# Kernel tuning notes

Hardware: AMD Instinct MI355X
Metric: run time of the kernel (lower is better)

Reference implementation:

```python
import jax, jax.numpy as jnp
import numpy as np

SEQ_LEN = 2048
EMBED_DIM = 1024
NUM_HEADS = 16
DIM_HEAD = EMBED_DIM // NUM_HEADS
BATCH = 4


def setup_inputs() -> dict:
    key = jax.random.key(0)
    k1, k2, k3 = jax.random.split(key, 3)
    x = jax.random.normal(k1, (SEQ_LEN, BATCH, EMBED_DIM), dtype=jnp.float32)
    weight_qkv = jax.random.normal(k2, (3 * EMBED_DIM, EMBED_DIM), dtype=jnp.float32) * (EMBED_DIM ** -0.5)
    weight_out = jax.random.normal(k3, (EMBED_DIM, EMBED_DIM), dtype=jnp.float32) * (EMBED_DIM ** -0.5)
    # causal mask: True where attention is DISALLOWED (strict upper triangle)
    mask = ~jnp.tril(jnp.ones((SEQ_LEN, SEQ_LEN), dtype=bool))[None, None]  # [1,1,L,L]
    return {"x": x, "weight_qkv": weight_qkv, "weight_out": weight_out, "mask": mask}


def reference(x, weight_qkv, weight_out, mask):
    L, N, E = x.shape
    H, Dh = NUM_HEADS, DIM_HEAD
    scale = Dh ** -0.5
    qkv = x @ weight_qkv.T                       # [L, N, 3E]
    q, k, v = jnp.split(qkv, 3, axis=-1)         # each [L, N, E]
    # [L, N, E] -> [N*H, L, Dh]
    def to_heads(t):
        return t.reshape(L, N * H, Dh).transpose(1, 0, 2)
    q, k, v = to_heads(q) * scale, to_heads(k), to_heads(v)
    attn = jnp.einsum('bld,bmd->blm', q, k)      # [N*H, L, L]
    attn = attn.reshape(N, H, L, L)
    attn = jnp.where(mask, jnp.float32(-100000.0), attn)
    attn = jax.nn.softmax(attn.reshape(N * H, L, L), axis=-1)
    out = jnp.einsum('blm,bmd->bld', attn, v)    # [N*H, L, Dh]
    out = out.transpose(1, 0, 2).reshape(L, N, E)
    return out @ weight_out.T
```

## Files before the change

kernel.cpp:

```cpp
#include <hip/hip_runtime.h>
#include <hip/hip_bf16.h>
#include <stdint.h>

constexpr int L  = 2048;
constexpr int NB = 4;
constexpr int E  = 1024;
constexpr int H  = 16;
constexpr int M  = L * NB;
constexpr int K  = E;
constexpr int QKV_LD = 3 * E;

typedef float  f32x4  __attribute__((ext_vector_type(4)));
typedef float  f32x16 __attribute__((ext_vector_type(16)));
typedef __bf16 bf16x4 __attribute__((ext_vector_type(4)));
typedef __bf16 bf16x8 __attribute__((ext_vector_type(8)));

#define AS1 __attribute__((address_space(1)))
#define AS3 __attribute__((address_space(3)))

static __device__ __forceinline__ void gl_lds16(const void* g, void* l) {
  __builtin_amdgcn_global_load_lds((const AS1 uint32_t*)g, (AS3 uint32_t*)l, 16, 0, 0);
}

__global__ __launch_bounds__(256)
void cvt_f32_bf16(const float* __restrict__ in, __bf16* __restrict__ out, int n4) {
  const int i = blockIdx.x * blockDim.x + threadIdx.x;
  if (i < n4) {
    const f32x4 v = ((const f32x4*)in)[i];
    bf16x4 o;
#pragma unroll
    for (int j = 0; j < 4; j++) o[j] = (__bf16)v[j];
    ((bf16x4*)out)[i] = o;
  }
}

template<int NC, typename OutT>
__global__ __launch_bounds__(256)
void gemm_bt(const __bf16* __restrict__ A, const __bf16* __restrict__ B,
             OutT* __restrict__ C) {
  constexpr int BK = 64;
  __shared__ char lds[2 * 128 * BK * 2];
  char* aL = lds;
  char* bL = lds + 128 * BK * 2;

  const int t    = threadIdx.x;
  const int lane = t & 63;
  const int w    = t >> 6;
  const int g    = lane >> 4;
  const int c    = lane & 15;

  const int nwg = gridDim.x * gridDim.y;
  const int lin = blockIdx.x + gridDim.x * blockIdx.y;
  const int q8  = nwg >> 3;
  const int swz = (lin & 7) * q8 + (lin >> 3);
  const int bx  = swz % gridDim.x;
  const int by  = swz / gridDim.x;

  const int rowBase = by * 128;
  const int colBase = bx * 128;

  const int srow = t >> 3;
  const int scb  = (t & 7) * 16;
  const int ssw  = scb ^ ((srow & 7) << 4);

  const char* aSrcBase = (const char*)(A + (size_t)(rowBase + srow) * K) + ssw;
  const char* bSrcBase = (const char*)(B + (size_t)(colBase + srow) * K) + ssw;

  f32x4 acc[4][4];
#pragma unroll
  for (int i = 0; i < 4; i++)
#pragma unroll
    for (int j = 0; j < 4; j++) acc[i][j] = f32x4{0.f, 0.f, 0.f, 0.f};

  const int wr = (w >> 1) * 64;
  const int wc = (w & 1) * 64;

  for (int k0 = 0; k0 < K; k0 += BK) {
    __syncthreads();
#pragma unroll
    for (int q = 0; q < 4; q++) {
      gl_lds16(aSrcBase + (size_t)2 * k0 + (size_t)q * 32 * K * 2, aL + q * 4096 + t * 16);
      gl_lds16(bSrcBase + (size_t)2 * k0 + (size_t)q * 32 * K * 2, bL + q * 4096 + t * 16);
    }
    __syncthreads();

    bf16x8 af[4][2], bfR[4][2];
#pragma unroll
    for (int mi = 0; mi < 4; mi++) {
      const int row = wr + mi * 16 + c;
      const int sw  = (row & 7) << 4;
#pragma unroll
      for (int ks = 0; ks < 2; ks++)
        af[mi][ks] = *(const bf16x8*)(aL + row * 128 + ((ks * 64 + g * 16) ^ sw));
    }
#pragma unroll
    for (int ni = 0; ni < 4; ni++) {
      const int row = wc + ni * 16 + c;
      const int sw  = (row & 7) << 4;
#pragma unroll
      for (int ks = 0; ks < 2; ks++)
        bfR[ni][ks] = *(const bf16x8*)(bL + row * 128 + ((ks * 64 + g * 16) ^ sw));
    }
#pragma unroll
    for (int mi = 0; mi < 4; mi++)
#pragma unroll
      for (int ni = 0; ni < 4; ni++)
#pragma unroll
        for (int ks = 0; ks < 2; ks++)
          acc[mi][ni] = __builtin_amdgcn_mfma_f32_16x16x32_bf16(
              af[mi][ks], bfR[ni][ks], acc[mi][ni], 0, 0, 0);
  }

#pragma unroll
  for (int mi = 0; mi < 4; mi++)
#pragma unroll
    for (int ni = 0; ni < 4; ni++)
#pragma unroll
      for (int r = 0; r < 4; r++) {
        const int row = rowBase + wr + mi * 16 + g * 4 + r;
        const int col = colBase + wc + ni * 16 + c;
        C[(size_t)row * NC + col] = (OutT)acc[mi][ni][r];
      }
}

__global__ __launch_bounds__(256)
void transpose_v(const __bf16* __restrict__ qkv, __bf16* __restrict__ vT) {
  __shared__ char tile[64 * 160];
  const int lt = blockIdx.x;
  const int bh = blockIdx.y;
  const int n  = bh >> 4, h = bh & 15;
  const int t  = threadIdx.x;
  const int r8 = t >> 3;
  const int c8 = (t & 7) * 8;

#pragma unroll
  for (int q2 = 0; q2 < 2; q2++) {
    const int l = q2 * 32 + r8;
    const bf16x8 v = *(const bf16x8*)(qkv + (size_t)((lt * 64 + l) * 4 + n) * QKV_LD +
                                      2 * E + h * 64 + c8);
    *(bf16x8*)(tile + l * 160 + ((c8 * 2) ^ (((l >> 3) & 7) << 4))) = v;
  }
  __syncthreads();
#pragma unroll
  for (int q2 = 0; q2 < 2; q2++) {
    const int d = q2 * 32 + r8;
    bf16x8 o;
#pragma unroll
    for (int i = 0; i < 8; i++) {
      const int l = c8 + i;
      o[i] = *(const __bf16*)(tile + l * 160 + ((d * 2) ^ (((l >> 3) & 7) << 4)));
    }
    *(bf16x8*)(vT + ((size_t)bh * 64 + d) * 2048 + lt * 64 + c8) = o;
  }
}

__global__ __launch_bounds__(256)
void attn_kernel(const __bf16* __restrict__ qkv, const __bf16* __restrict__ vT,
                 __bf16* __restrict__ out) {
  const int b  = blockIdx.x;
  const int qx = blockIdx.y;
  const int n  = b >> 4;
  const int h  = b & 15;

  __shared__ char kl[2][64 * 128];
  __shared__ char vl[2][64 * 128];
  __shared__ char pl[4][32 * 128];

  const int t    = threadIdx.x;
  const int lane = t & 63;
  const int w    = t >> 6;
  const int l31  = lane & 31;
  const int hi   = lane >> 5;

  const int srow = t >> 3;
  const int scb  = (t & 7) * 16;
  int kssw[2];
#pragma unroll
  for (int q2 = 0; q2 < 2; q2++) {
    const int row = q2 * 32 + srow;
    kssw[q2] = scb ^ (((row ^ (row >> 3)) & 7) << 4);
  }

  const int krow0 = l31,      sw0 = ((krow0 ^ (krow0 >> 3)) & 7) << 4;
  const int krow1 = 32 + l31, sw1 = ((krow1 ^ (krow1 >> 3)) & 7) << 4;

  constexpr float QSCALE = 0.125f * 1.4426950408889634f;

  const int qt    = (w < 2) ? qx : 31 - qx;
  const int qh    = w & 1;
  const int ktEnd = 31 - qx;
  const int qg    = qt * 64 + qh * 32 + l31;

  char* pw = pl[w];

  bf16x8 qb[4];
  {
    const __bf16* qp = qkv + (size_t)(qg * 4 + n) * QKV_LD + h * 64;
#pragma unroll
    for (int ds = 0; ds < 4; ds++) {
      qb[ds] = *(const bf16x8*)(qp + ds * 16 + hi * 8);
#pragma unroll
      for (int i = 0; i < 8; i++) qb[ds][i] = (__bf16)((float)qb[ds][i] * QSCALE);
    }
  }

  float m_c = -3e38f, l_c = 0.f;
  f32x16 o0, o1;
#pragma unroll
  for (int j = 0; j < 16; j++) { o0[j] = 0.f; o1[j] = 0.f; }

  int cur = 0;

#pragma unroll
  for (int q2 = 0; q2 < 2; q2++) {
    const int kvrow = q2 * 32 + srow;
    gl_lds16((const char*)(qkv + (size_t)(kvrow * 4 + n) * QKV_LD + E + h * 64) + kssw[q2],
             kl[0] + q2 * 4096 + t * 16);
    gl_lds16((const char*)(vT + ((size_t)b * 64 + kvrow) * 2048) + kssw[q2],
             vl[0] + q2 * 4096 + t * 16);
  }

  for (int kt = 0; kt <= ktEnd; ++kt) {
    __syncthreads();

    if (kt < ktEnd) {
      const int nx = kt + 1;
#pragma unroll
      for (int q2 = 0; q2 < 2; q2++) {
        const int kvrow = nx * 64 + q2 * 32 + srow;
        gl_lds16((const char*)(qkv + (size_t)(kvrow * 4 + n) * QKV_LD + E + h * 64) + kssw[q2],
                 kl[cur ^ 1] + q2 * 4096 + t * 16);
        const int vd = q2 * 32 + srow;
        gl_lds16((const char*)(vT + ((size_t)b * 64 + vd) * 2048 + nx * 64) + kssw[q2],
                 vl[cur ^ 1] + q2 * 4096 + t * 16);
      }
    }
    __builtin_amdgcn_sched_barrier(0);

    if (kt <= qt) {
      const char* klc = kl[cur];
      const char* vlc = vl[cur];

      f32x16 s0, s1;
#pragma unroll
      for (int j = 0; j < 16; j++) { s0[j] = 0.f; s1[j] = 0.f; }
      __builtin_amdgcn_s_setprio(1);
#pragma unroll
      for (int ds = 0; ds < 4; ds++) {
        const int col = ds * 32 + hi * 16;
        const bf16x8 ka0 = *(const bf16x8*)(klc + krow0 * 128 + (col ^ sw0));
        const bf16x8 ka1 = *(const bf16x8*)(klc + krow1 * 128 + (col ^ sw1));
        s0 = __builtin_amdgcn_mfma_f32_32x32x16_bf16(ka0, qb[ds], s0, 0, 0, 0);
        s1 = __builtin_amdgcn_mfma_f32_32x32x16_bf16(ka1, qb[ds], s1, 0, 0, 0);
      }
      __builtin_amdgcn_s_setprio(0);

      if (kt == qt) {
#pragma unroll
        for (int reg = 0; reg < 16; reg++) {
          const int kvp = (reg & 3) + 8 * (reg >> 2) + 4 * hi;
          if (kt * 64 + kvp      > qg) s0[reg] = -1e30f;
          if (kt * 64 + 32 + kvp > qg) s1[reg] = -1e30f;
        }
      }

      float rmax = s0[0];
#pragma unroll
      for (int reg = 1; reg < 16; reg++) rmax = fmaxf(rmax, s0[reg]);
#pragma unroll
      for (int reg = 0; reg < 16; reg++) rmax = fmaxf(rmax, s1[reg]);
      rmax = fmaxf(rmax, __shfl_xor(rmax, 32));

      if (__any(rmax > m_c + 8.f)) {
        const float mnew  = fmaxf(m_c, rmax);
        const float alpha = exp2f(m_c - mnew);
        l_c *= alpha;
#pragma unroll
        for (int reg = 0; reg < 16; reg++) {
          const int   qp = (reg & 3) + 8 * (reg >> 2) + 4 * hi;
          const float ar = __shfl(alpha, qp);
          o0[reg] *= ar;
          o1[reg] *= ar;
        }
        m_c = mnew;
      }

      float rsum = 0.f;
#pragma unroll
      for (int reg = 0; reg < 16; reg++) {
        const float e0 = exp2f(s0[reg] - m_c);
        const float e1 = exp2f(s1[reg] - m_c);
        s0[reg] = e0; s1[reg] = e1;
        rsum += e0 + e1;
      }
      rsum += __shfl_xor(rsum, 32);
      l_c += rsum;

#pragma unroll
      for (int rg = 0; rg < 8; rg++) {
        bf16x4 pk;
#pragma unroll
        for (int j = 0; j < 4; j++)
          pk[j] = (__bf16)((rg < 4) ? s0[(rg & 3) * 4 + j] : s1[(rg & 3) * 4 + j]);
        const int kvb = (rg & 3) * 16 + hi * 8 + (rg >> 2) * 64;
        *(bf16x4*)(pw + l31 * 128 + (kvb ^ sw0)) = pk;
      }

#pragma unroll
      for (int s_ = 0; s_ < 4; s_++) {
        const int colp = s_ * 32 + hi * 16;
        const bf16x8 pa  = *(const bf16x8*)(pw + l31 * 128 + (colp ^ sw0));
        const bf16x8 vb0 = *(const bf16x8*)(vlc + krow0 * 128 + (colp ^ sw0));
        const bf16x8 vb1 = *(const bf16x8*)(vlc + krow1 * 128 + (colp ^ sw1));
        __builtin_amdgcn_s_setprio(1);
        o0 = __builtin_amdgcn_mfma_f32_32x32x16_bf16(pa, vb0, o0, 0, 0, 0);
        o1 = __builtin_amdgcn_mfma_f32_32x32x16_bf16(pa, vb1, o1, 0, 0, 0);
        __builtin_amdgcn_s_setprio(0);
      }
    }

    cur ^= 1;
  }

  const float inv = 1.f / l_c;
#pragma unroll
  for (int reg = 0; reg < 16; reg++) {
    const int   qp  = (reg & 3) + 8 * (reg >> 2) + 4 * hi;
    const float li  = __shfl(inv, qp);
    const int   qrw = qt * 64 + qh * 32 + qp;
    const size_t base = (size_t)(qrw * 4 + n) * E + h * 64;
    out[base + l31]      = (__bf16)(o0[reg] * li);
    out[base + 32 + l31] = (__bf16)(o1[reg] * li);
  }
}

extern "C" void kernel_launch(void* const* d_in, const int* in_sizes, int n_in,
                              void* d_out, int out_size, void* d_ws, size_t ws_size,
                              hipStream_t stream) {
  const float* x    = (const float*)d_in[0];
  const float* wqkv = (const float*)d_in[1];
  const float* wout = (const float*)d_in[2];

  char* ws = (char*)d_ws;
  __bf16* x_bf    = (__bf16*)ws;                         ws += (size_t)M * E * 2;
  __bf16* wqkv_bf = (__bf16*)ws;                         ws += (size_t)QKV_LD * E * 2;
  __bf16* wout_bf = (__bf16*)ws;                         ws += (size_t)E * E * 2;
  __bf16* qkv     = (__bf16*)ws;                         ws += (size_t)M * QKV_LD * 2;
  __bf16* attno   = (__bf16*)ws;
  __bf16* vT      = x_bf;
  float*  outp    = (float*)d_out;

  cvt_f32_bf16<<<(M * E / 4) / 256, 256, 0, stream>>>(x, x_bf, M * E / 4);
  cvt_f32_bf16<<<(QKV_LD * E / 4) / 256, 256, 0, stream>>>(wqkv, wqkv_bf, QKV_LD * E / 4);
  cvt_f32_bf16<<<(E * E / 4) / 256, 256, 0, stream>>>(wout, wout_bf, E * E / 4);

  gemm_bt<QKV_LD, __bf16><<<dim3(QKV_LD / 128, M / 128), 256, 0, stream>>>(x_bf, wqkv_bf, qkv);
  transpose_v<<<dim3(L / 64, NB * H), 256, 0, stream>>>(qkv, vT);
  attn_kernel<<<dim3(NB * H, 16), 256, 0, stream>>>(qkv, vT, attno);
  gemm_bt<E, float><<<dim3(E / 128, M / 128), 256, 0, stream>>>(attno, wout_bf, outp);
}
```

Before: 218.9 us.

## Share K/V tiles across four warps on 128-row query blocks and shuffle P via registers

The attention kernel now gives each block two passes over 128-row query supertiles (y and 15-y), so all four warps work on adjacent query rows and share every loaded K/V tile instead of splitting between two distant 64-row tiles. The grid halves to 8 blocks per head. The softmax probability tile is no longer staged through shared memory; it is rearranged into the MFMA A-operand layout with cross-half-wave shuffles. This cuts redundant K/V loads and LDS traffic, but leaves fewer, longer blocks with a serialized second pass and adds shuffle instructions.

New measurement: 199.0 us. 1.1x faster.

```diff
diff --git a/kernel.cpp b/kernel.cpp
--- a/kernel.cpp
+++ b/kernel.cpp
@@ -14,6 +14,8 @@
 typedef float  f32x16 __attribute__((ext_vector_type(16)));
 typedef __bf16 bf16x4 __attribute__((ext_vector_type(4)));
 typedef __bf16 bf16x8 __attribute__((ext_vector_type(8)));
+typedef unsigned int uint2v __attribute__((ext_vector_type(2)));
+typedef unsigned int uint4v __attribute__((ext_vector_type(4)));
 
 #define AS1 __attribute__((address_space(1)))
 #define AS3 __attribute__((address_space(3)))
@@ -158,13 +160,12 @@
 void attn_kernel(const __bf16* __restrict__ qkv, const __bf16* __restrict__ vT,
                  __bf16* __restrict__ out) {
   const int b  = blockIdx.x;
-  const int qx = blockIdx.y;
+  const int y  = blockIdx.y;
   const int n  = b >> 4;
   const int h  = b & 15;
 
   __shared__ char kl[2][64 * 128];
   __shared__ char vl[2][64 * 128];
-  __shared__ char pl[4][32 * 128];
 
   const int t    = threadIdx.x;
   const int lane = t & 63;
@@ -185,29 +186,6 @@
   const int krow1 = 32 + l31, sw1 = ((krow1 ^ (krow1 >> 3)) & 7) << 4;
 
   constexpr float QSCALE = 0.125f * 1.4426950408889634f;
-
-  const int qt    = (w < 2) ? qx : 31 - qx;
-  const int qh    = w & 1;
-  const int ktEnd = 31 - qx;
-  const int qg    = qt * 64 + qh * 32 + l31;
-
-  char* pw = pl[w];
-
-  bf16x8 qb[4];
-  {
-    const __bf16* qp = qkv + (size_t)(qg * 4 + n) * QKV_LD + h * 64;
-#pragma unroll
-    for (int ds = 0; ds < 4; ds++) {
-      qb[ds] = *(const bf16x8*)(qp + ds * 16 + hi * 8);
-#pragma unroll
-      for (int i = 0; i < 8; i++) qb[ds][i] = (__bf16)((float)qb[ds][i] * QSCALE);
-    }
-  }
-
-  float m_c = -3e38f, l_c = 0.f;
-  f32x16 o0, o1;
-#pragma unroll
-  for (int j = 0; j < 16; j++) { o0[j] = 0.f; o1[j] = 0.f; }
 
   int cur = 0;
 
@@ -220,117 +198,152 @@
              vl[0] + q2 * 4096 + t * 16);
   }
 
-  for (int kt = 0; kt <= ktEnd; ++kt) {
-    __syncthreads();
-
-    if (kt < ktEnd) {
-      const int nx = kt + 1;
-#pragma unroll
-      for (int q2 = 0; q2 < 2; q2++) {
-        const int kvrow = nx * 64 + q2 * 32 + srow;
-        gl_lds16((const char*)(qkv + (size_t)(kvrow * 4 + n) * QKV_LD + E + h * 64) + kssw[q2],
-                 kl[cur ^ 1] + q2 * 4096 + t * 16);
-        const int vd = q2 * 32 + srow;
-        gl_lds16((const char*)(vT + ((size_t)b * 64 + vd) * 2048 + nx * 64) + kssw[q2],
-                 vl[cur ^ 1] + q2 * 4096 + t * 16);
+  for (int pass = 0; pass < 2; ++pass) {
+    const int qsup = pass ? 15 - y : y;
+    const int qb_  = qsup * 128 + w * 32;
+    const int qg   = qb_ + l31;
+    const int ktEnd = 2 * qsup + 1;
+
+    bf16x8 qb[4];
+    {
+      const __bf16* qp = qkv + (size_t)(qg * 4 + n) * QKV_LD + h * 64;
+#pragma unroll
+      for (int ds = 0; ds < 4; ds++) {
+        qb[ds] = *(const bf16x8*)(qp + ds * 16 + hi * 8);
+#pragma unroll
+        for (int i = 0; i < 8; i++) qb[ds][i] = (__bf16)((float)qb[ds][i] * QSCALE);
       }
     }
-    __builtin_amdgcn_sched_barrier(0);
-
-    if (kt <= qt) {
-      const char* klc = kl[cur];
-      const char* vlc = vl[cur];
-
-      f32x16 s0, s1;
-#pragma unroll
-      for (int j = 0; j < 16; j++) { s0[j] = 0.f; s1[j] = 0.f; }
-      __builtin_amdgcn_s_setprio(1);
-#pragma unroll
-      for (int ds = 0; ds < 4; ds++) {
-        const int col = ds * 32 + hi * 16;
-        const bf16x8 ka0 = *(const bf16x8*)(klc + krow0 * 128 + (col ^ sw0));
-        const bf16x8 ka1 = *(const bf16x8*)(klc + krow1 * 128 + (col ^ sw1));
-        s0 = __builtin_amdgcn_mfma_f32_32x32x16_bf16(ka0, qb[ds], s0, 0, 0, 0);
-        s1 = __builtin_amdgcn_mfma_f32_32x32x16_bf16(ka1, qb[ds], s1, 0, 0, 0);
+
+    float m_c = -3e38f, l_c = 0.f;
+    f32x16 o0, o1;
+#pragma unroll
+    for (int j = 0; j < 16; j++) { o0[j] = 0.f; o1[j] = 0.f; }
+
+    for (int kt = 0; kt <= ktEnd; ++kt) {
+      __syncthreads();
+
+      const bool last = (kt == ktEnd);
+      if (!last || pass == 0) {
+        const int nx = last ? 0 : kt + 1;
+#pragma unroll
+        for (int q2 = 0; q2 < 2; q2++) {
+          const int kvrow = nx * 64 + q2 * 32 + srow;
+          gl_lds16((const char*)(qkv + (size_t)(kvrow * 4 + n) * QKV_LD + E + h * 64) + kssw[q2],
+                   kl[cur ^ 1] + q2 * 4096 + t * 16);
+          const int vd = q2 * 32 + srow;
+          gl_lds16((const char*)(vT + ((size_t)b * 64 + vd) * 2048 + nx * 64) + kssw[q2],
+                   vl[cur ^ 1] + q2 * 4096 + t * 16);
+        }
       }
-      __builtin_amdgcn_s_setprio(0);
-
-      if (kt == qt) {
+      __builtin_amdgcn_sched_barrier(0);
+
+      if (kt * 64 <= qb_ + 31) {
+        const char* klc = kl[cur];
+        const char* vlc = vl[cur];
+
+        f32x16 s0, s1;
+#pragma unroll
+        for (int j = 0; j < 16; j++) { s0[j] = 0.f; s1[j] = 0.f; }
+        __builtin_amdgcn_s_setprio(1);
+#pragma unroll
+        for (int ds = 0; ds < 4; ds++) {
+          const int col = ds * 32 + hi * 16;
+          const bf16x8 ka0 = *(const bf16x8*)(klc + krow0 * 128 + (col ^ sw0));
+          const bf16x8 ka1 = *(const bf16x8*)(klc + krow1 * 128 + (col ^ sw1));
+          s0 = __builtin_amdgcn_mfma_f32_32x32x16_bf16(ka0, qb[ds], s0, 0, 0, 0);
+          s1 = __builtin_amdgcn_mfma_f32_32x32x16_bf16(ka1, qb[ds], s1, 0, 0, 0);
+        }
+        __builtin_amdgcn_s_setprio(0);
+
+        if (kt * 64 + 63 > qb_) {
+#pragma unroll
+          for (int reg = 0; reg < 16; reg++) {
+            const int kvp = (reg & 3) + 8 * (reg >> 2) + 4 * hi;
+            if (kt * 64 + kvp      > qg) s0[reg] = -1e30f;
+            if (kt * 64 + 32 + kvp > qg) s1[reg] = -1e30f;
+          }
+        }
+
+        float rmax = s0[0];
+#pragma unroll
+        for (int reg = 1; reg < 16; reg++) rmax = fmaxf(rmax, s0[reg]);
+#pragma unroll
+        for (int reg = 0; reg < 16; reg++) rmax = fmaxf(rmax, s1[reg]);
+        rmax = fmaxf(rmax, __shfl_xor(rmax, 32));
+
+        if (__any(rmax > m_c + 8.f)) {
+          const float mnew  = fmaxf(m_c, rmax);
+          const float alpha = exp2f(m_c - mnew);
+          l_c *= alpha;
+#pragma unroll
+          for (int reg = 0; reg < 16; reg++) {
+            const int   qp = (reg & 3) + 8 * (reg >> 2) + 4 * hi;
+            const float ar = __shfl(alpha, qp);
+            o0[reg] *= ar;
+            o1[reg] *= ar;
+          }
+          m_c = mnew;
+        }
+
+        float rsum = 0.f;
 #pragma unroll
         for (int reg = 0; reg < 16; reg++) {
-          const int kvp = (reg & 3) + 8 * (reg >> 2) + 4 * hi;
-          if (kt * 64 + kvp      > qg) s0[reg] = -1e30f;
-          if (kt * 64 + 32 + kvp > qg) s1[reg] = -1e30f;
+          const float e0 = exp2f(s0[reg] - m_c);
+          const float e1 = exp2f(s1[reg] - m_c);
+          s0[reg] = e0; s1[reg] = e1;
+          rsum += e0 + e1;
+        }
+        rsum += __shfl_xor(rsum, 32);
+        l_c += rsum;
+
+        unsigned int runA[8], runB[8];
+#pragma unroll
+        for (int rg = 0; rg < 8; rg++) {
+          bf16x4 pk;
+#pragma unroll
+          for (int j = 0; j < 4; j++)
+            pk[j] = (__bf16)((rg < 4) ? s0[(rg & 3) * 4 + j] : s1[(rg & 3) * 4 + j]);
+          const uint2v u = *(const uint2v*)&pk;
+          runA[rg] = u[0]; runB[rg] = u[1];
+        }
+
+#pragma unroll
+        for (int s_ = 0; s_ < 4; s_++) {
+          const unsigned int ownA = hi ? runA[2 * s_ + 1] : runA[2 * s_];
+          const unsigned int ownB = hi ? runB[2 * s_ + 1] : runB[2 * s_];
+          const unsigned int sndA = hi ? runA[2 * s_]     : runA[2 * s_ + 1];
+          const unsigned int sndB = hi ? runB[2 * s_]     : runB[2 * s_ + 1];
+          const unsigned int rxA  = (unsigned int)__shfl_xor((int)sndA, 32);
+          const unsigned int rxB  = (unsigned int)__shfl_xor((int)sndB, 32);
+          uint4v pu;
+          pu[0] = hi ? rxA : ownA;  pu[1] = hi ? rxB : ownB;
+          pu[2] = hi ? ownA : rxA;  pu[3] = hi ? ownB : rxB;
+          const bf16x8 pa = *(const bf16x8*)&pu;
+
+          const int colp = s_ * 32 + hi * 16;
+          const bf16x8 vb0 = *(const bf16x8*)(vlc + krow0 * 128 + (colp ^ sw0));
+          const bf16x8 vb1 = *(const bf16x8*)(vlc + krow1 * 128 + (colp ^ sw1));
+          __builtin_amdgcn_s_setprio(1);
+          o0 = __builtin_amdgcn_mfma_f32_32x32x16_bf16(pa, vb0, o0, 0, 0, 0);
+          o1 = __builtin_amdgcn_mfma_f32_32x32x16_bf16(pa, vb1, o1, 0, 0, 0);
+          __builtin_amdgcn_s_setprio(0);
         }
       }
 
-      float rmax = s0[0];
-#pragma unroll
-      for (int reg = 1; reg < 16; reg++) rmax = fmaxf(rmax, s0[reg]);
-#pragma unroll
-      for (int reg = 0; reg < 16; reg++) rmax = fmaxf(rmax, s1[reg]);
-      rmax = fmaxf(rmax, __shfl_xor(rmax, 32));
-
-      if (__any(rmax > m_c + 8.f)) {
-        const float mnew  = fmaxf(m_c, rmax);
-        const float alpha = exp2f(m_c - mnew);
-        l_c *= alpha;
-#pragma unroll
-        for (int reg = 0; reg < 16; reg++) {
-          const int   qp = (reg & 3) + 8 * (reg >> 2) + 4 * hi;
-          const float ar = __shfl(alpha, qp);
-          o0[reg] *= ar;
-          o1[reg] *= ar;
-        }
-        m_c = mnew;
-      }
-
-      float rsum = 0.f;
-#pragma unroll
-      for (int reg = 0; reg < 16; reg++) {
-        const float e0 = exp2f(s0[reg] - m_c);
-        const float e1 = exp2f(s1[reg] - m_c);
-        s0[reg] = e0; s1[reg] = e1;
-        rsum += e0 + e1;
-      }
-      rsum += __shfl_xor(rsum, 32);
-      l_c += rsum;
-
-#pragma unroll
-      for (int rg = 0; rg < 8; rg++) {
-        bf16x4 pk;
-#pragma unroll
-        for (int j = 0; j < 4; j++)
-          pk[j] = (__bf16)((rg < 4) ? s0[(rg & 3) * 4 + j] : s1[(rg & 3) * 4 + j]);
-        const int kvb = (rg & 3) * 16 + hi * 8 + (rg >> 2) * 64;
-        *(bf16x4*)(pw + l31 * 128 + (kvb ^ sw0)) = pk;
-      }
-
-#pragma unroll
-      for (int s_ = 0; s_ < 4; s_++) {
-        const int colp = s_ * 32 + hi * 16;
-        const bf16x8 pa  = *(const bf16x8*)(pw + l31 * 128 + (colp ^ sw0));
-        const bf16x8 vb0 = *(const bf16x8*)(vlc + krow0 * 128 + (colp ^ sw0));
-        const bf16x8 vb1 = *(const bf16x8*)(vlc + krow1 * 128 + (colp ^ sw1));
-        __builtin_amdgcn_s_setprio(1);
-        o0 = __builtin_amdgcn_mfma_f32_32x32x16_bf16(pa, vb0, o0, 0, 0, 0);
-        o1 = __builtin_amdgcn_mfma_f32_32x32x16_bf16(pa, vb1, o1, 0, 0, 0);
-        __builtin_amdgcn_s_setprio(0);
-      }
-    }
-
-    cur ^= 1;
-  }
-
-  const float inv = 1.f / l_c;
-#pragma unroll
-  for (int reg = 0; reg < 16; reg++) {
-    const int   qp  = (reg & 3) + 8 * (reg >> 2) + 4 * hi;
-    const float li  = __shfl(inv, qp);
-    const int   qrw = qt * 64 + qh * 32 + qp;
-    const size_t base = (size_t)(qrw * 4 + n) * E + h * 64;
-    out[base + l31]      = (__bf16)(o0[reg] * li);
-    out[base + 32 + l31] = (__bf16)(o1[reg] * li);
+      cur ^= 1;
+    }
+
+    const float inv = 1.f / l_c;
+#pragma unroll
+    for (int reg = 0; reg < 16; reg++) {
+      const int   qp  = (reg & 3) + 8 * (reg >> 2) + 4 * hi;
+      const float li  = __shfl(inv, qp);
+      const int   qrw = qb_ + qp;
+      const size_t base = (size_t)(qrw * 4 + n) * E + h * 64;
+      out[base + l31]      = (__bf16)(o0[reg] * li);
+      out[base + 32 + l31] = (__bf16)(o1[reg] * li);
+    }
   }
 }
 
@@ -356,6 +369,6 @@
 
   gemm_bt<QKV_LD, __bf16><<<dim3(QKV_LD / 128, M / 128), 256, 0, stream>>>(x_bf, wqkv_bf, qkv);
   transpose_v<<<dim3(L / 64, NB * H), 256, 0, stream>>>(qkv, vT);
-  attn_kernel<<<dim3(NB * H, 16), 256, 0, stream>>>(qkv, vT, attno);
+  attn_kernel<<<dim3(NB * H, 8), 256, 0, stream>>>(qkv, vT, attno);
   gemm_bt<E, float><<<dim3(E / 128, M / 128), 256, 0, stream>>>(attno, wout_bf, outp);
 }
```
